# Kernel tuning notes

Measured on AMD Instinct MI355X. Metric: run time of the kernel, lower is better.

Reference implementation:

```python
import jax, jax.numpy as jnp
import numpy as np

N = 30000       # nodes
E = 480000      # edges (before self loops)
IN = 128        # in_channels
H1, C1 = 5, 64  # conv1 heads, per-head channels
OUT = 64        # out_channels (conv2, heads=1)
PE = 100000     # pos/neg edges for decode
NEG_SLOPE = 0.2


def setup_inputs() -> dict:
    key = jax.random.key(0)
    ks = jax.random.split(key, 12)
    return {
        "x": jax.random.normal(ks[0], (N, IN), dtype=jnp.float32),
        "edge_index": jax.random.randint(ks[1], (2, E), 0, N),
        "pos_edge_index": jax.random.randint(ks[2], (2, PE), 0, N),
        "neg_edge_index": jax.random.randint(ks[3], (2, PE), 0, N),
        "W1": jax.random.normal(ks[4], (IN, H1 * C1), dtype=jnp.float32) * 0.05,
        "att_src1": jax.random.normal(ks[5], (H1, C1), dtype=jnp.float32) * 0.1,
        "att_dst1": jax.random.normal(ks[6], (H1, C1), dtype=jnp.float32) * 0.1,
        "b1": jnp.zeros((H1 * C1,), dtype=jnp.float32),
        "W2": jax.random.normal(ks[7], (H1 * C1, OUT), dtype=jnp.float32) * 0.05,
        "att_src2": jax.random.normal(ks[8], (1, OUT), dtype=jnp.float32) * 0.1,
        "att_dst2": jax.random.normal(ks[9], (1, OUT), dtype=jnp.float32) * 0.1,
        "b2": jnp.zeros((OUT,), dtype=jnp.float32),
    }


def gat_conv(x, edge_index, W, att_src, att_dst, bias, heads, out_ch):
    """PyG GATConv: add self loops, linear proj, edge softmax, scatter-sum, concat heads."""
    n = x.shape[0]
    loops = jnp.arange(n)
    src = jnp.concatenate([edge_index[0], loops])  # message sources j
    dst = jnp.concatenate([edge_index[1], loops])  # message targets i
    h = (x @ W).reshape(n, heads, out_ch)          # [N,H,C]
    a_src = jnp.sum(h * att_src, axis=-1)          # [N,H]
    a_dst = jnp.sum(h * att_dst, axis=-1)          # [N,H]
    e = jax.nn.leaky_relu(a_src[src] + a_dst[dst], NEG_SLOPE)  # [E',H]
    # numerically-stable segment softmax over incoming edges of each dst node
    m = jax.ops.segment_max(e, dst, num_segments=n)
    m = jax.lax.stop_gradient(jnp.where(jnp.isfinite(m), m, 0.0))
    ex = jnp.exp(e - m[dst])
    s = jax.ops.segment_sum(ex, dst, num_segments=n)
    alpha = ex / (s[dst] + 1e-16)                  # [E',H]
    out = jax.ops.segment_sum(alpha[:, :, None] * h[src], dst, num_segments=n)  # [N,H,C]
    return out.reshape(n, heads * out_ch) + bias


def reference(x, edge_index, pos_edge_index, neg_edge_index,
              W1, att_src1, att_dst1, b1, W2, att_src2, att_dst2, b2):
    z = gat_conv(x, edge_index, W1, att_src1, att_dst1, b1, H1, C1)
    z = jax.nn.relu(z)
    z = gat_conv(z, edge_index, W2, att_src2, att_dst2, b2, 1, OUT)
    ei = jnp.concatenate([pos_edge_index, neg_edge_index], axis=-1)
    return jnp.sum(z[ei[0]] * z[ei[1]], axis=-1)  # [2*PE]
```

## Files before the change

kernel.cpp:

```cpp
#include <hip/hip_runtime.h>
#include <hip/hip_fp16.h>
#include <cstdint>
#include <cstddef>
#include <type_traits>

#define N_NODES 30000
#define N_EDGES 480000
#define N_EDGES_SL (N_EDGES + N_NODES)
#define IN_CH 128
#define HEADS1 5
#define C1 64
#define D1 (HEADS1 * C1)
#define OUT_CH 64
#define PE_CNT 100000
#define NEG_SLOPE 0.2f
#define BCAP 64
#define GEMM1_BLOCKS 469
#define BUCKET_BLOCKS 128

typedef _Float16 f16x8 __attribute__((ext_vector_type(8)));
typedef _Float16 f16x2 __attribute__((ext_vector_type(2)));
typedef float fx4 __attribute__((ext_vector_type(4)));

#if defined(__has_builtin)
#if __has_builtin(__builtin_amdgcn_fdot2)
#define HAS_FDOT2 1
#endif
#endif

static __device__ __forceinline__ float leaky(float x) {
    return fmaxf(x, NEG_SLOPE * x);
}

template<int NH, typename AT>
static __device__ __forceinline__ void gemm_phase(const AT* __restrict__ A,
                                                  const __half* __restrict__ Wt,
                                                  __half* __restrict__ C, int K,
                                                  const float* __restrict__ att_src,
                                                  const float* __restrict__ att_dst,
                                                  float* __restrict__ as_out,
                                                  float* __restrict__ ad_out,
                                                  int slot, int nsl, int lane) {
    const int N = NH * 64;
    int q = lane >> 4, l16 = lane & 15;
    for (int tile = slot; tile < N_NODES / 16; tile += nsl) {
        int rowBase = tile * 16;
        int arow = rowBase + l16;
        fx4 zero4 = {0.f, 0.f, 0.f, 0.f};
        fx4 acc[NH][4];
#pragma unroll
        for (int h = 0; h < NH; ++h)
#pragma unroll
            for (int c = 0; c < 4; ++c) acc[h][c] = zero4;
        for (int kk = 0; kk < K; kk += 32) {
            f16x8 af;
            if constexpr (std::is_same<AT, float>::value) {
                const float4* s = (const float4*)(A + (size_t)arow * K + kk + q * 8);
                float4 v0 = s[0], v1 = s[1];
                af[0] = (_Float16)v0.x; af[1] = (_Float16)v0.y;
                af[2] = (_Float16)v0.z; af[3] = (_Float16)v0.w;
                af[4] = (_Float16)v1.x; af[5] = (_Float16)v1.y;
                af[6] = (_Float16)v1.z; af[7] = (_Float16)v1.w;
            } else {
                af = *(const f16x8*)((const __half*)A + (size_t)arow * K + kk + q * 8);
            }
#pragma unroll
            for (int h = 0; h < NH; ++h) {
#pragma unroll
                for (int c = 0; c < 4; ++c) {
                    int col = h * 64 + c * 16 + l16;
                    f16x8 bf = *(const f16x8*)(Wt + (size_t)col * K + kk + q * 8);
                    acc[h][c] = __builtin_amdgcn_mfma_f32_16x16x32_f16(af, bf, acc[h][c], 0, 0, 0);
                }
            }
        }
#pragma unroll
        for (int h = 0; h < NH; ++h) {
            float ps[4] = {0.f, 0.f, 0.f, 0.f};
            float pd[4] = {0.f, 0.f, 0.f, 0.f};
#pragma unroll
            for (int c = 0; c < 4; ++c) {
                int gcol = h * 64 + c * 16 + l16;
                float av = att_src[gcol];
                float dv = att_dst[gcol];
#pragma unroll
                for (int reg = 0; reg < 4; ++reg) {
                    int grow = rowBase + q * 4 + reg;
                    float val = acc[h][c][reg];
                    C[(size_t)grow * N + gcol] = __float2half(val);
                    ps[reg] += val * av;
                    pd[reg] += val * dv;
                }
            }
#pragma unroll
            for (int off = 1; off < 16; off <<= 1) {
#pragma unroll
                for (int reg = 0; reg < 4; ++reg) {
                    ps[reg] += __shfl_xor(ps[reg], off, 64);
                    pd[reg] += __shfl_xor(pd[reg], off, 64);
                }
            }
            if (l16 == 0) {
#pragma unroll
                for (int reg = 0; reg < 4; ++reg) {
                    int grow = rowBase + q * 4 + reg;
                    as_out[(size_t)h * N_NODES + grow] = ps[reg];
                    ad_out[(size_t)h * N_NODES + grow] = pd[reg];
                }
            }
        }
    }
}

__global__ __launch_bounds__(256) void k_init(int* __restrict__ cnt,
                                              int* __restrict__ esrc2,
                                              const float* __restrict__ W1,
                                              __half* __restrict__ Wt1,
                                              const float* __restrict__ W2,
                                              __half* __restrict__ Wt2) {
    int t = blockIdx.x * 256 + threadIdx.x;
    int nthr = gridDim.x * 256;
    for (int i = t; i < N_NODES + 8; i += nthr) cnt[i] = (i < N_NODES) ? 1 : 0;
    for (int i = t; i < N_NODES; i += nthr) esrc2[i * BCAP] = i;
    const int T1 = IN_CH * D1, T2 = D1 * OUT_CH;
    for (int idx = t; idx < T1 + T2; idx += nthr) {
        if (idx < T1) {
            int k = idx / D1, n = idx - k * D1;
            Wt1[(size_t)n * IN_CH + k] = __float2half(W1[idx]);
        } else {
            int i2 = idx - T1;
            int k = i2 / OUT_CH, n = i2 - k * OUT_CH;
            Wt2[(size_t)n * D1 + k] = __float2half(W2[i2]);
        }
    }
}

__global__ __launch_bounds__(256) void k_build_gemm1(const int* __restrict__ edge,
                                                     int* __restrict__ cnt,
                                                     int* __restrict__ esrc2,
                                                     int* __restrict__ ovf_cnt,
                                                     int* __restrict__ ovf,
                                                     const float* __restrict__ x,
                                                     const __half* __restrict__ Wt1,
                                                     __half* __restrict__ h1,
                                                     const float* __restrict__ att_src1,
                                                     const float* __restrict__ att_dst1,
                                                     float* __restrict__ as1,
                                                     float* __restrict__ ad1) {
    int lane = threadIdx.x & 63, wv = threadIdx.x >> 6;
    if (blockIdx.x < GEMM1_BLOCKS) {
        gemm_phase<HEADS1, float>(x, Wt1, h1, IN_CH, att_src1, att_dst1, as1, ad1,
                                  blockIdx.x * 4 + wv, GEMM1_BLOCKS * 4, lane);
    } else {
        int t = (blockIdx.x - GEMM1_BLOCKS) * 256 + threadIdx.x;
        const int nthr = BUCKET_BLOCKS * 256;
        int e = t;
        for (; e + 3 * nthr < N_EDGES; e += 4 * nthr) {
            int e1 = e + nthr, e2 = e + 2 * nthr, e3 = e + 3 * nthr;
            int s0 = edge[e];  int d0 = edge[N_EDGES + e];
            int s1 = edge[e1]; int d1 = edge[N_EDGES + e1];
            int s2 = edge[e2]; int d2 = edge[N_EDGES + e2];
            int s3 = edge[e3]; int d3 = edge[N_EDGES + e3];
            int r0 = atomicAdd(&cnt[d0], 1);
            int r1 = atomicAdd(&cnt[d1], 1);
            int r2 = atomicAdd(&cnt[d2], 1);
            int r3 = atomicAdd(&cnt[d3], 1);
            if (r0 < BCAP) esrc2[d0 * BCAP + r0] = s0;
            else { int oi = atomicAdd(ovf_cnt, 1); ovf[2 * oi] = d0; ovf[2 * oi + 1] = s0; }
            if (r1 < BCAP) esrc2[d1 * BCAP + r1] = s1;
            else { int oi = atomicAdd(ovf_cnt, 1); ovf[2 * oi] = d1; ovf[2 * oi + 1] = s1; }
            if (r2 < BCAP) esrc2[d2 * BCAP + r2] = s2;
            else { int oi = atomicAdd(ovf_cnt, 1); ovf[2 * oi] = d2; ovf[2 * oi + 1] = s2; }
            if (r3 < BCAP) esrc2[d3 * BCAP + r3] = s3;
            else { int oi = atomicAdd(ovf_cnt, 1); ovf[2 * oi] = d3; ovf[2 * oi + 1] = s3; }
        }
        for (; e < N_EDGES; e += nthr) {
            int s = edge[e];
            int d = edge[N_EDGES + e];
            int r = atomicAdd(&cnt[d], 1);
            if (r < BCAP) {
                esrc2[d * BCAP + r] = s;
            } else {
                int oi = atomicAdd(ovf_cnt, 1);
                ovf[2 * oi] = d;
                ovf[2 * oi + 1] = s;
            }
        }
    }
}

template<int NH, bool RELU>
__global__ __launch_bounds__(256) void k_attn_agg(const int* __restrict__ cnt,
                                                  const int* __restrict__ esrc2,
                                                  const int* __restrict__ ovf_cnt,
                                                  const int* __restrict__ ovf,
                                                  const __half* __restrict__ hf,
                                                  const float* __restrict__ a_src,
                                                  const float* __restrict__ a_dst,
                                                  const float* __restrict__ bias,
                                                  __half* __restrict__ zout) {
    __shared__ unsigned wpk[4][64];
    __shared__ int jbuf[4][64];
    __shared__ float red[4][584];
    int wid = (blockIdx.x * 256 + threadIdx.x) >> 6;
    int lane = threadIdx.x & 63;
    int wv = threadIdx.x >> 6;
    if (wid >= N_NODES * NH) return;
    int h = wid / N_NODES;
    int node = wid - h * N_NODES;
    int deg = cnt[node];
    const float* asrc_h = a_src + (size_t)h * N_NODES;
    float adst = a_dst[(size_t)h * N_NODES + node];
    const int RS = NH * 64;
    if (deg <= BCAP) {
        int es = lane >> 3, cg = lane & 7;
        const __half* hbase = hf + h * 64 + cg * 8;
        int joff = 0;
        float ex = 0.f;
        if (lane < deg) {
            int j = esrc2[node * BCAP + lane];
            joff = j * RS;
            ex = __expf(leaky(asrc_h[j] + adst));
        }
        float s = ex;
#pragma unroll
        for (int off = 1; off < 64; off <<= 1)
            s += __shfl_xor(s, off, 64);
        float r = 1.f / (s + 1e-16f);
        __half2 wn = __float2half2_rn(ex * r);
        wpk[wv][lane] = *(unsigned*)&wn;
        jbuf[wv][lane] = joff;
        __half2 acch[4] = {__half2{0, 0}, __half2{0, 0}, __half2{0, 0}, __half2{0, 0}};
        for (int k0 = 0; k0 < deg; k0 += 32) {
            int kA = k0 + es, kB = kA + 8, kC = kA + 16, kD = kA + 24;
            unsigned uA = wpk[wv][kA];
            unsigned uB = wpk[wv][kB];
            unsigned uC = wpk[wv][kC];
            unsigned uD = wpk[wv][kD];
            int jA = jbuf[wv][kA];
            int jB = jbuf[wv][kB];
            int jC = jbuf[wv][kC];
            int jD = jbuf[wv][kD];
            float4 vA = *(const float4*)(hbase + jA);
            float4 vB = *(const float4*)(hbase + jB);
            float4 vC = *(const float4*)(hbase + jC);
            float4 vD = *(const float4*)(hbase + jD);
            __half2 hwA = *(__half2*)&uA, hwB = *(__half2*)&uB;
            __half2 hwC = *(__half2*)&uC, hwD = *(__half2*)&uD;
            const __half2* pA = (const __half2*)&vA;
            const __half2* pB = (const __half2*)&vB;
            const __half2* pC = (const __half2*)&vC;
            const __half2* pD = (const __half2*)&vD;
#pragma unroll
            for (int i = 0; i < 4; ++i) {
                acch[i] = __hfma2(pA[i], hwA, acch[i]);
                acch[i] = __hfma2(pB[i], hwB, acch[i]);
                acch[i] = __hfma2(pC[i], hwC, acch[i]);
                acch[i] = __hfma2(pD[i], hwD, acch[i]);
            }
        }
#pragma unroll
        for (int i = 0; i < 4; ++i) {
            float2 f = __half22float2(acch[i]);
            red[wv][(cg * 8 + 2 * i) * 9 + es] = f.x;
            red[wv][(cg * 8 + 2 * i + 1) * 9 + es] = f.y;
        }
        float tot = 0.f;
#pragma unroll
        for (int e2 = 0; e2 < 8; ++e2)
            tot += red[wv][lane * 9 + e2];
        float o = tot + bias[h * 64 + lane];
        if (RELU) o = fmaxf(o, 0.f);
        zout[(size_t)node * RS + h * 64 + lane] = __float2half(o);
    } else {
        int ovn = *ovf_cnt;
        float s = __expf(leaky(asrc_h[esrc2[node * BCAP + lane]] + adst));
#pragma unroll
        for (int off = 1; off < 64; off <<= 1)
            s += __shfl_xor(s, off, 64);
        float s2 = 0.f;
        for (int k = lane; k < ovn; k += 64)
            if (ovf[2 * k] == node)
                s2 += __expf(leaky(asrc_h[ovf[2 * k + 1]] + adst));
#pragma unroll
        for (int off = 1; off < 64; off <<= 1)
            s2 += __shfl_xor(s2, off, 64);
        float r = 1.f / (s + s2 + 1e-16f);
        float a = 0.f;
        for (int k = 0; k < BCAP; ++k) {
            int j = esrc2[node * BCAP + k];
            float w = __expf(leaky(asrc_h[j] + adst));
            a += w * __half2float(hf[(size_t)j * RS + h * 64 + lane]);
        }
        for (int k = 0; k < ovn; ++k) {
            if (ovf[2 * k] == node) {
                int j = ovf[2 * k + 1];
                float w = __expf(leaky(asrc_h[j] + adst));
                a += w * __half2float(hf[(size_t)j * RS + h * 64 + lane]);
            }
        }
        float o = a * r + bias[h * 64 + lane];
        if (RELU) o = fmaxf(o, 0.f);
        zout[(size_t)node * RS + h * 64 + lane] = __float2half(o);
    }
}

__global__ __launch_bounds__(256) void k_gemm2(const __half* __restrict__ z1,
                                               const __half* __restrict__ Wt2,
                                               __half* __restrict__ h2,
                                               const float* __restrict__ att_src2,
                                               const float* __restrict__ att_dst2,
                                               float* __restrict__ as2,
                                               float* __restrict__ ad2) {
    int lane = threadIdx.x & 63, wv = threadIdx.x >> 6;
    gemm_phase<1, __half>(z1, Wt2, h2, D1, att_src2, att_dst2, as2, ad2,
                          blockIdx.x * 4 + wv, gridDim.x * 4, lane);
}

__global__ __launch_bounds__(256) void k_decode(const int* __restrict__ pos,
                                                const int* __restrict__ neg,
                                                const __half* __restrict__ z2,
                                                float* __restrict__ out) {
    int t = blockIdx.x * 256 + threadIdx.x;
    int e = t >> 3;
    int lc = t & 7;
    if (e >= 2 * PE_CNT) return;
    int a, b;
    if (e < PE_CNT) { a = pos[e]; b = pos[PE_CNT + e]; }
    else { int k = e - PE_CNT; a = neg[k]; b = neg[PE_CNT + k]; }
    union U { float4 f; f16x2 h[4]; __half2 hh[4]; } ua, ub;
    ua.f = *(const float4*)(z2 + (size_t)a * OUT_CH + lc * 8);
    ub.f = *(const float4*)(z2 + (size_t)b * OUT_CH + lc * 8);
    float v = 0.f;
#pragma unroll
    for (int i = 0; i < 4; ++i) {
#ifdef HAS_FDOT2
        v = __builtin_amdgcn_fdot2(ua.h[i], ub.h[i], v, false);
#else
        float2 fa = __half22float2(ua.hh[i]);
        float2 fb = __half22float2(ub.hh[i]);
        v += fa.x * fb.x + fa.y * fb.y;
#endif
    }
#pragma unroll
    for (int off = 1; off < 8; off <<= 1)
        v += __shfl_xor(v, off, 64);
    if (lc == 0) out[e] = v;
}

extern "C" void kernel_launch(void* const* d_in, const int* in_sizes, int n_in,
                              void* d_out, int out_size, void* d_ws, size_t ws_size,
                              hipStream_t stream) {
    const float* x        = (const float*)d_in[0];
    const int* edge_index = (const int*)d_in[1];
    const int* pos_ei     = (const int*)d_in[2];
    const int* neg_ei     = (const int*)d_in[3];
    const float* W1       = (const float*)d_in[4];
    const float* att_src1 = (const float*)d_in[5];
    const float* att_dst1 = (const float*)d_in[6];
    const float* b1       = (const float*)d_in[7];
    const float* W2       = (const float*)d_in[8];
    const float* att_src2 = (const float*)d_in[9];
    const float* att_dst2 = (const float*)d_in[10];
    const float* b2       = (const float*)d_in[11];
    float* out            = (float*)d_out;

    char* ws = (char*)d_ws;
    size_t off = 0;
    auto alloc = [&](size_t bytes) -> void* {
        void* p = ws + off;
        off = (off + bytes + 255) & ~(size_t)255;
        return p;
    };
    int* cnt     = (int*)alloc(sizeof(int) * (N_NODES + 8));
    int* ovfc    = cnt + N_NODES;
    int* esrc2   = (int*)alloc(sizeof(int) * (size_t)N_NODES * BCAP);
    int* ovf     = (int*)alloc(sizeof(int) * (size_t)2 * N_EDGES_SL);
    __half* h1   = (__half*)alloc(sizeof(__half) * (size_t)N_NODES * D1);
    __half* z1   = (__half*)alloc(sizeof(__half) * (size_t)N_NODES * D1);
    __half* h2   = (__half*)alloc(sizeof(__half) * (size_t)N_NODES * OUT_CH);
    __half* z2   = (__half*)alloc(sizeof(__half) * (size_t)N_NODES * OUT_CH);
    __half* Wt1  = (__half*)alloc(sizeof(__half) * (size_t)D1 * IN_CH);
    __half* Wt2  = (__half*)alloc(sizeof(__half) * (size_t)OUT_CH * D1);
    float* as1   = (float*)alloc(sizeof(float) * (size_t)N_NODES * HEADS1);
    float* ad1   = (float*)alloc(sizeof(float) * (size_t)N_NODES * HEADS1);
    float* as2   = (float*)alloc(sizeof(float) * (size_t)N_NODES);
    float* ad2   = (float*)alloc(sizeof(float) * (size_t)N_NODES);

    k_init<<<240, 256, 0, stream>>>(cnt, esrc2, W1, Wt1, W2, Wt2);
    k_build_gemm1<<<GEMM1_BLOCKS + BUCKET_BLOCKS, 256, 0, stream>>>(
        edge_index, cnt, esrc2, ovfc, ovf, x, Wt1, h1, att_src1, att_dst1, as1, ad1);
    k_attn_agg<HEADS1, true><<<(N_NODES * HEADS1 + 3) / 4, 256, 0, stream>>>(
        cnt, esrc2, ovfc, ovf, h1, as1, ad1, b1, z1);
    k_gemm2<<<469, 256, 0, stream>>>(z1, Wt2, h2, att_src2, att_dst2, as2, ad2);
    k_attn_agg<1, false><<<(N_NODES + 3) / 4, 256, 0, stream>>>(
        cnt, esrc2, ovfc, ovf, h2, as2, ad2, b2, z2);
    k_decode<<<(2 * PE_CNT * 8 + 255) / 256, 256, 0, stream>>>(pos_ei, neg_ei, z2, out);

    (void)in_sizes; (void)n_in; (void)out_size; (void)ws_size;
}
```

Baseline: 224.3 us.

## Process all heads per wave in attention aggregation, pad counters, node-major scores

New measurement: 208.3 us. -7.1%, faster.

```diff
diff --git a/kernel.cpp b/kernel.cpp
--- a/kernel.cpp
+++ b/kernel.cpp
@@ -15,6 +15,7 @@
 #define PE_CNT 100000
 #define NEG_SLOPE 0.2f
 #define BCAP 64
+#define CPAD 32
 #define GEMM1_BLOCKS 469
 #define BUCKET_BLOCKS 128
 
@@ -32,7 +33,7 @@
     return fmaxf(x, NEG_SLOPE * x);
 }
 
-template<int NH, typename AT>
+template<int NH, int SP, typename AT>
 static __device__ __forceinline__ void gemm_phase(const AT* __restrict__ A,
                                                   const __half* __restrict__ Wt,
                                                   __half* __restrict__ C, int K,
@@ -104,8 +105,8 @@
 #pragma unroll
                 for (int reg = 0; reg < 4; ++reg) {
                     int grow = rowBase + q * 4 + reg;
-                    as_out[(size_t)h * N_NODES + grow] = ps[reg];
-                    ad_out[(size_t)h * N_NODES + grow] = pd[reg];
+                    as_out[(size_t)grow * SP + h] = ps[reg];
+                    ad_out[(size_t)grow * SP + h] = pd[reg];
                 }
             }
         }
@@ -113,6 +114,7 @@
 }
 
 __global__ __launch_bounds__(256) void k_init(int* __restrict__ cnt,
+                                              int* __restrict__ ovfc,
                                               int* __restrict__ esrc2,
                                               const float* __restrict__ W1,
                                               __half* __restrict__ Wt1,
@@ -120,8 +122,11 @@
                                               __half* __restrict__ Wt2) {
     int t = blockIdx.x * 256 + threadIdx.x;
     int nthr = gridDim.x * 256;
-    for (int i = t; i < N_NODES + 8; i += nthr) cnt[i] = (i < N_NODES) ? 1 : 0;
-    for (int i = t; i < N_NODES; i += nthr) esrc2[i * BCAP] = i;
+    for (int i = t; i < N_NODES; i += nthr) {
+        cnt[(size_t)i * CPAD] = 1;
+        esrc2[i * BCAP] = i;
+    }
+    if (t == 0) *ovfc = 0;
     const int T1 = IN_CH * D1, T2 = D1 * OUT_CH;
     for (int idx = t; idx < T1 + T2; idx += nthr) {
         if (idx < T1) {
@@ -149,8 +154,8 @@
                                                      float* __restrict__ ad1) {
     int lane = threadIdx.x & 63, wv = threadIdx.x >> 6;
     if (blockIdx.x < GEMM1_BLOCKS) {
-        gemm_phase<HEADS1, float>(x, Wt1, h1, IN_CH, att_src1, att_dst1, as1, ad1,
-                                  blockIdx.x * 4 + wv, GEMM1_BLOCKS * 4, lane);
+        gemm_phase<HEADS1, 8, float>(x, Wt1, h1, IN_CH, att_src1, att_dst1, as1, ad1,
+                                     blockIdx.x * 4 + wv, GEMM1_BLOCKS * 4, lane);
     } else {
         int t = (blockIdx.x - GEMM1_BLOCKS) * 256 + threadIdx.x;
         const int nthr = BUCKET_BLOCKS * 256;
@@ -161,10 +166,10 @@
             int s1 = edge[e1]; int d1 = edge[N_EDGES + e1];
             int s2 = edge[e2]; int d2 = edge[N_EDGES + e2];
             int s3 = edge[e3]; int d3 = edge[N_EDGES + e3];
-            int r0 = atomicAdd(&cnt[d0], 1);
-            int r1 = atomicAdd(&cnt[d1], 1);
-            int r2 = atomicAdd(&cnt[d2], 1);
-            int r3 = atomicAdd(&cnt[d3], 1);
+            int r0 = atomicAdd(&cnt[(size_t)d0 * CPAD], 1);
+            int r1 = atomicAdd(&cnt[(size_t)d1 * CPAD], 1);
+            int r2 = atomicAdd(&cnt[(size_t)d2 * CPAD], 1);
+            int r3 = atomicAdd(&cnt[(size_t)d3 * CPAD], 1);
             if (r0 < BCAP) esrc2[d0 * BCAP + r0] = s0;
             else { int oi = atomicAdd(ovf_cnt, 1); ovf[2 * oi] = d0; ovf[2 * oi + 1] = s0; }
             if (r1 < BCAP) esrc2[d1 * BCAP + r1] = s1;
@@ -177,7 +182,7 @@
         for (; e < N_EDGES; e += nthr) {
             int s = edge[e];
             int d = edge[N_EDGES + e];
-            int r = atomicAdd(&cnt[d], 1);
+            int r = atomicAdd(&cnt[(size_t)d * CPAD], 1);
             if (r < BCAP) {
                 esrc2[d * BCAP + r] = s;
             } else {
@@ -199,109 +204,140 @@
                                                   const float* __restrict__ a_dst,
                                                   const float* __restrict__ bias,
                                                   __half* __restrict__ zout) {
-    __shared__ unsigned wpk[4][64];
+    const int SP = (NH == 1) ? 1 : 8;
+    __shared__ unsigned wpk[4][NH][64];
     __shared__ int jbuf[4][64];
     __shared__ float red[4][584];
-    int wid = (blockIdx.x * 256 + threadIdx.x) >> 6;
+    int node = (blockIdx.x * 256 + threadIdx.x) >> 6;
     int lane = threadIdx.x & 63;
     int wv = threadIdx.x >> 6;
-    if (wid >= N_NODES * NH) return;
-    int h = wid / N_NODES;
-    int node = wid - h * N_NODES;
-    int deg = cnt[node];
-    const float* asrc_h = a_src + (size_t)h * N_NODES;
-    float adst = a_dst[(size_t)h * N_NODES + node];
+    if (node >= N_NODES) return;
+    int deg = cnt[(size_t)node * CPAD];
     const int RS = NH * 64;
+    float da[NH];
+    if constexpr (NH == 1) {
+        da[0] = a_dst[node];
+    } else {
+        float4 d0 = *(const float4*)(a_dst + (size_t)node * SP);
+        da[0] = d0.x; da[1] = d0.y; da[2] = d0.z; da[3] = d0.w;
+        da[4] = a_dst[(size_t)node * SP + 4];
+    }
     if (deg <= BCAP) {
         int es = lane >> 3, cg = lane & 7;
-        const __half* hbase = hf + h * 64 + cg * 8;
         int joff = 0;
-        float ex = 0.f;
+        float e[NH];
+#pragma unroll
+        for (int h = 0; h < NH; ++h) e[h] = 0.f;
         if (lane < deg) {
             int j = esrc2[node * BCAP + lane];
             joff = j * RS;
-            ex = __expf(leaky(asrc_h[j] + adst));
-        }
-        float s = ex;
-#pragma unroll
-        for (int off = 1; off < 64; off <<= 1)
-            s += __shfl_xor(s, off, 64);
-        float r = 1.f / (s + 1e-16f);
-        __half2 wn = __float2half2_rn(ex * r);
-        wpk[wv][lane] = *(unsigned*)&wn;
+            if constexpr (NH == 1) {
+                e[0] = __expf(leaky(a_src[j] + da[0]));
+            } else {
+                float4 s0 = *(const float4*)(a_src + (size_t)j * SP);
+                float s4 = a_src[(size_t)j * SP + 4];
+                e[0] = __expf(leaky(s0.x + da[0]));
+                e[1] = __expf(leaky(s0.y + da[1]));
+                e[2] = __expf(leaky(s0.z + da[2]));
+                e[3] = __expf(leaky(s0.w + da[3]));
+                e[4] = __expf(leaky(s4 + da[4]));
+            }
+        }
+        float s[NH];
+#pragma unroll
+        for (int h = 0; h < NH; ++h) s[h] = e[h];
+#pragma unroll
+        for (int off = 1; off < 64; off <<= 1) {
+#pragma unroll
+            for (int h = 0; h < NH; ++h) s[h] += __shfl_xor(s[h], off, 64);
+        }
+#pragma unroll
+        for (int h = 0; h < NH; ++h) {
+            float r = 1.f / (s[h] + 1e-16f);
+            __half2 wn = __float2half2_rn(e[h] * r);
+            wpk[wv][h][lane] = *(unsigned*)&wn;
+        }
         jbuf[wv][lane] = joff;
-        __half2 acch[4] = {__half2{0, 0}, __half2{0, 0}, __half2{0, 0}, __half2{0, 0}};
-        for (int k0 = 0; k0 < deg; k0 += 32) {
-            int kA = k0 + es, kB = kA + 8, kC = kA + 16, kD = kA + 24;
-            unsigned uA = wpk[wv][kA];
-            unsigned uB = wpk[wv][kB];
-            unsigned uC = wpk[wv][kC];
-            unsigned uD = wpk[wv][kD];
-            int jA = jbuf[wv][kA];
-            int jB = jbuf[wv][kB];
-            int jC = jbuf[wv][kC];
-            int jD = jbuf[wv][kD];
-            float4 vA = *(const float4*)(hbase + jA);
-            float4 vB = *(const float4*)(hbase + jB);
-            float4 vC = *(const float4*)(hbase + jC);
-            float4 vD = *(const float4*)(hbase + jD);
-            __half2 hwA = *(__half2*)&uA, hwB = *(__half2*)&uB;
-            __half2 hwC = *(__half2*)&uC, hwD = *(__half2*)&uD;
-            const __half2* pA = (const __half2*)&vA;
-            const __half2* pB = (const __half2*)&vB;
-            const __half2* pC = (const __half2*)&vC;
-            const __half2* pD = (const __half2*)&vD;
+#pragma unroll
+        for (int h = 0; h < NH; ++h) {
+            const __half* hbase = hf + h * 64 + cg * 8;
+            __half2 acch[4] = {__half2{0, 0}, __half2{0, 0}, __half2{0, 0}, __half2{0, 0}};
+            for (int k0 = 0; k0 < deg; k0 += 32) {
+                int kA = k0 + es, kB = kA + 8, kC = kA + 16, kD = kA + 24;
+                unsigned uA = wpk[wv][h][kA];
+                unsigned uB = wpk[wv][h][kB];
+                unsigned uC = wpk[wv][h][kC];
+                unsigned uD = wpk[wv][h][kD];
+                int jA = jbuf[wv][kA];
+                int jB = jbuf[wv][kB];
+                int jC = jbuf[wv][kC];
+                int jD = jbuf[wv][kD];
+                float4 vA = *(const float4*)(hbase + jA);
+                float4 vB = *(const float4*)(hbase + jB);
+                float4 vC = *(const float4*)(hbase + jC);
+                float4 vD = *(const float4*)(hbase + jD);
+                __half2 hwA = *(__half2*)&uA, hwB = *(__half2*)&uB;
+                __half2 hwC = *(__half2*)&uC, hwD = *(__half2*)&uD;
+                const __half2* pA = (const __half2*)&vA;
+                const __half2* pB = (const __half2*)&vB;
+                const __half2* pC = (const __half2*)&vC;
+                const __half2* pD = (const __half2*)&vD;
+#pragma unroll
+                for (int i = 0; i < 4; ++i) {
+                    acch[i] = __hfma2(pA[i], hwA, acch[i]);
+                    acch[i] = __hfma2(pB[i], hwB, acch[i]);
+                    acch[i] = __hfma2(pC[i], hwC, acch[i]);
+                    acch[i] = __hfma2(pD[i], hwD, acch[i]);
+                }
+            }
 #pragma unroll
             for (int i = 0; i < 4; ++i) {
-                acch[i] = __hfma2(pA[i], hwA, acch[i]);
-                acch[i] = __hfma2(pB[i], hwB, acch[i]);
-                acch[i] = __hfma2(pC[i], hwC, acch[i]);
-                acch[i] = __hfma2(pD[i], hwD, acch[i]);
-            }
-        }
-#pragma unroll
-        for (int i = 0; i < 4; ++i) {
-            float2 f = __half22float2(acch[i]);
-            red[wv][(cg * 8 + 2 * i) * 9 + es] = f.x;
-            red[wv][(cg * 8 + 2 * i + 1) * 9 + es] = f.y;
-        }
-        float tot = 0.f;
-#pragma unroll
-        for (int e2 = 0; e2 < 8; ++e2)
-            tot += red[wv][lane * 9 + e2];
-        float o = tot + bias[h * 64 + lane];
-        if (RELU) o = fmaxf(o, 0.f);
-        zout[(size_t)node * RS + h * 64 + lane] = __float2half(o);
+                float2 f = __half22float2(acch[i]);
+                red[wv][(cg * 8 + 2 * i) * 9 + es] = f.x;
+                red[wv][(cg * 8 + 2 * i + 1) * 9 + es] = f.y;
+            }
+            float tot = 0.f;
+#pragma unroll
+            for (int e2 = 0; e2 < 8; ++e2)
+                tot += red[wv][lane * 9 + e2];
+            float o = tot + bias[h * 64 + lane];
+            if (RELU) o = fmaxf(o, 0.f);
+            zout[(size_t)node * RS + h * 64 + lane] = __float2half(o);
+        }
     } else {
         int ovn = *ovf_cnt;
-        float s = __expf(leaky(asrc_h[esrc2[node * BCAP + lane]] + adst));
-#pragma unroll
-        for (int off = 1; off < 64; off <<= 1)
-            s += __shfl_xor(s, off, 64);
-        float s2 = 0.f;
-        for (int k = lane; k < ovn; k += 64)
-            if (ovf[2 * k] == node)
-                s2 += __expf(leaky(asrc_h[ovf[2 * k + 1]] + adst));
-#pragma unroll
-        for (int off = 1; off < 64; off <<= 1)
-            s2 += __shfl_xor(s2, off, 64);
-        float r = 1.f / (s + s2 + 1e-16f);
-        float a = 0.f;
-        for (int k = 0; k < BCAP; ++k) {
-            int j = esrc2[node * BCAP + k];
-            float w = __expf(leaky(asrc_h[j] + adst));
-            a += w * __half2float(hf[(size_t)j * RS + h * 64 + lane]);
-        }
-        for (int k = 0; k < ovn; ++k) {
-            if (ovf[2 * k] == node) {
-                int j = ovf[2 * k + 1];
-                float w = __expf(leaky(asrc_h[j] + adst));
+#pragma unroll
+        for (int h = 0; h < NH; ++h) {
+            float adsth = da[h];
+            float sden = __expf(leaky(a_src[(size_t)esrc2[node * BCAP + lane] * SP + h] + adsth));
+#pragma unroll
+            for (int off = 1; off < 64; off <<= 1)
+                sden += __shfl_xor(sden, off, 64);
+            float s2 = 0.f;
+            for (int k = lane; k < ovn; k += 64)
+                if (ovf[2 * k] == node)
+                    s2 += __expf(leaky(a_src[(size_t)ovf[2 * k + 1] * SP + h] + adsth));
+#pragma unroll
+            for (int off = 1; off < 64; off <<= 1)
+                s2 += __shfl_xor(s2, off, 64);
+            float r = 1.f / (sden + s2 + 1e-16f);
+            float a = 0.f;
+            for (int k = 0; k < BCAP; ++k) {
+                int j = esrc2[node * BCAP + k];
+                float w = __expf(leaky(a_src[(size_t)j * SP + h] + adsth));
                 a += w * __half2float(hf[(size_t)j * RS + h * 64 + lane]);
             }
-        }
-        float o = a * r + bias[h * 64 + lane];
-        if (RELU) o = fmaxf(o, 0.f);
-        zout[(size_t)node * RS + h * 64 + lane] = __float2half(o);
+            for (int k = 0; k < ovn; ++k) {
+                if (ovf[2 * k] == node) {
+                    int j = ovf[2 * k + 1];
+                    float w = __expf(leaky(a_src[(size_t)j * SP + h] + adsth));
+                    a += w * __half2float(hf[(size_t)j * RS + h * 64 + lane]);
+                }
+            }
+            float o = a * r + bias[h * 64 + lane];
+            if (RELU) o = fmaxf(o, 0.f);
+            zout[(size_t)node * RS + h * 64 + lane] = __float2half(o);
+        }
     }
 }
 
@@ -313,8 +349,8 @@
                                                float* __restrict__ as2,
                                                float* __restrict__ ad2) {
     int lane = threadIdx.x & 63, wv = threadIdx.x >> 6;
-    gemm_phase<1, __half>(z1, Wt2, h2, D1, att_src2, att_dst2, as2, ad2,
-                          blockIdx.x * 4 + wv, gridDim.x * 4, lane);
+    gemm_phase<1, 1, __half>(z1, Wt2, h2, D1, att_src2, att_dst2, as2, ad2,
+                             blockIdx.x * 4 + wv, gridDim.x * 4, lane);
 }
 
 __global__ __launch_bounds__(256) void k_decode(const int* __restrict__ pos,
@@ -372,8 +408,8 @@
         off = (off + bytes + 255) & ~(size_t)255;
         return p;
     };
-    int* cnt     = (int*)alloc(sizeof(int) * (N_NODES + 8));
-    int* ovfc    = cnt + N_NODES;
+    int* cnt     = (int*)alloc(sizeof(int) * (size_t)N_NODES * CPAD);
+    int* ovfc    = (int*)alloc(sizeof(int) * 8);
     int* esrc2   = (int*)alloc(sizeof(int) * (size_t)N_NODES * BCAP);
     int* ovf     = (int*)alloc(sizeof(int) * (size_t)2 * N_EDGES_SL);
     __half* h1   = (__half*)alloc(sizeof(__half) * (size_t)N_NODES * D1);
@@ -382,15 +418,15 @@
     __half* z2   = (__half*)alloc(sizeof(__half) * (size_t)N_NODES * OUT_CH);
     __half* Wt1  = (__half*)alloc(sizeof(__half) * (size_t)D1 * IN_CH);
     __half* Wt2  = (__half*)alloc(sizeof(__half) * (size_t)OUT_CH * D1);
-    float* as1   = (float*)alloc(sizeof(float) * (size_t)N_NODES * HEADS1);
-    float* ad1   = (float*)alloc(sizeof(float) * (size_t)N_NODES * HEADS1);
+    float* as1   = (float*)alloc(sizeof(float) * (size_t)N_NODES * 8);
+    float* ad1   = (float*)alloc(sizeof(float) * (size_t)N_NODES * 8);
     float* as2   = (float*)alloc(sizeof(float) * (size_t)N_NODES);
     float* ad2   = (float*)alloc(sizeof(float) * (size_t)N_NODES);
 
-    k_init<<<240, 256, 0, stream>>>(cnt, esrc2, W1, Wt1, W2, Wt2);
+    k_init<<<240, 256, 0, stream>>>(cnt, ovfc, esrc2, W1, Wt1, W2, Wt2);
     k_build_gemm1<<<GEMM1_BLOCKS + BUCKET_BLOCKS, 256, 0, stream>>>(
         edge_index, cnt, esrc2, ovfc, ovf, x, Wt1, h1, att_src1, att_dst1, as1, ad1);
-    k_attn_agg<HEADS1, true><<<(N_NODES * HEADS1 + 3) / 4, 256, 0, stream>>>(
+    k_attn_agg<HEADS1, true><<<(N_NODES + 3) / 4, 256, 0, stream>>>(
         cnt, esrc2, ovfc, ovf, h1, as1, ad1, b1, z1);
     k_gemm2<<<469, 256, 0, stream>>>(z1, Wt2, h2, att_src2, att_dst2, as2, ad2);
     k_attn_agg<1, false><<<(N_NODES + 3) / 4, 256, 0, stream>>>(
```
